# Kernel optimization log

Hardware: AMD Instinct MI355X
Metric: run time of the kernel (lower is better)

Reference implementation:

```python
import jax, jax.numpy as jnp
import numpy as np

C_ATOM, C_Z, N_HEADS = 512, 64, 16
HEAD_DIM = C_ATOM // N_HEADS
EPS = 1e-5


def _layernorm(x, gamma, beta):
    mu = jnp.mean(x, axis=-1, keepdims=True)
    var = jnp.mean(jnp.square(x - mu), axis=-1, keepdims=True)
    return (x - mu) * jax.lax.rsqrt(var + EPS) * gamma + beta


def _adaln(x, cond, gamma, beta, pw, pb):
    # cond: [B, C] -> scale/shift: [B, 1, C]
    ss = cond @ pw.T + pb  # [B, 2C]
    scale, shift = jnp.split(ss[:, None, :], 2, axis=-1)
    return _layernorm(x, gamma, beta) * (1.0 + scale) + shift


def setup_inputs() -> dict:
    key = jax.random.key(0)
    ks = jax.random.split(key, 20)
    B, L = 2, 1024
    s = 1.0 / np.sqrt(C_ATOM)
    inp = {
        "x": jax.random.normal(ks[0], (B, L, C_ATOM), jnp.float32),
        "pair": jax.random.normal(ks[1], (B, L, L, C_Z), jnp.float32),
        "time_cond": jax.random.normal(ks[2], (B, C_ATOM), jnp.float32),
        "ln1_g": jnp.ones((C_ATOM,), jnp.float32),
        "ln1_b": jnp.zeros((C_ATOM,), jnp.float32),
        "ada1_w": jax.random.normal(ks[3], (2 * C_ATOM, C_ATOM), jnp.float32) * 0.02,
        "ada1_b": jnp.zeros((2 * C_ATOM,), jnp.float32),
        "wq": jax.random.normal(ks[4], (C_ATOM, C_ATOM), jnp.float32) * s,
        "wk": jax.random.normal(ks[5], (C_ATOM, C_ATOM), jnp.float32) * s,
        "wv": jax.random.normal(ks[6], (C_ATOM, C_ATOM), jnp.float32) * s,
        "w_pair": jax.random.normal(ks[7], (N_HEADS, C_Z), jnp.float32) * (1.0 / np.sqrt(C_Z)),
        "wo": jax.random.normal(ks[8], (C_ATOM, C_ATOM), jnp.float32) * s,
        "bo": jnp.zeros((C_ATOM,), jnp.float32),
        "ln2_g": jnp.ones((C_ATOM,), jnp.float32),
        "ln2_b": jnp.zeros((C_ATOM,), jnp.float32),
        "ada2_w": jax.random.normal(ks[9], (2 * C_ATOM, C_ATOM), jnp.float32) * 0.02,
        "ada2_b": jnp.zeros((2 * C_ATOM,), jnp.float32),
        "w1": jax.random.normal(ks[10], (4 * C_ATOM, C_ATOM), jnp.float32) * s,
        "b1": jnp.zeros((4 * C_ATOM,), jnp.float32),
        "w2": jax.random.normal(ks[11], (C_ATOM, 4 * C_ATOM), jnp.float32) * (1.0 / np.sqrt(4 * C_ATOM)),
        "b2": jnp.zeros((C_ATOM,), jnp.float32),
    }
    return inp


def reference(x, pair, time_cond, ln1_g, ln1_b, ada1_w, ada1_b, wq, wk, wv,
              w_pair, wo, bo, ln2_g, ln2_b, ada2_w, ada2_b, w1, b1, w2, b2):
    B, L, C = x.shape
    h = _adaln(x, time_cond, ln1_g, ln1_b, ada1_w, ada1_b)
    q = (h @ wq.T).reshape(B, L, N_HEADS, HEAD_DIM)
    k = (h @ wk.T).reshape(B, L, N_HEADS, HEAD_DIM)
    v = (h @ wv.T).reshape(B, L, N_HEADS, HEAD_DIM)
    attn = jnp.einsum('bihd,bjhd->bhij', q, k) / np.sqrt(HEAD_DIM)
    attn = attn + jnp.einsum('bijc,hc->bhij', pair, w_pair)  # additive pair bias
    attn = jax.nn.softmax(attn, axis=-1)
    out = jnp.einsum('bhij,bjhd->bihd', attn, v).reshape(B, L, C)
    x = x + out @ wo.T + bo
    h2 = _adaln(x, time_cond, ln2_g, ln2_b, ada2_w, ada2_b)
    ffn = jax.nn.gelu(h2 @ w1.T + b1, approximate=False) @ w2.T + b2
    return x + ffn
```

## Files before the change

### kernel.cpp

```cpp
#include <hip/hip_runtime.h>
#include <math.h>

typedef unsigned short u16;
typedef __attribute__((ext_vector_type(8))) short bf16x8;
typedef __attribute__((ext_vector_type(4))) short s16x4;
typedef __attribute__((ext_vector_type(4))) float f32x4;

__device__ __forceinline__ u16 f2bf(float f) {
  union { float f; unsigned u; } v; v.f = f;
  unsigned r = v.u + 0x7FFFu + ((v.u >> 16) & 1u);
  return (u16)(r >> 16);
}
__device__ __forceinline__ float bf2f(u16 h) {
  union { unsigned u; float f; } v; v.u = ((unsigned)h) << 16; return v.f;
}
__device__ __forceinline__ void gload_lds16(const void* g, void* l) {
  __builtin_amdgcn_global_load_lds((const __attribute__((address_space(1))) void*)g,
                                   (__attribute__((address_space(3))) void*)l, 16, 0, 0);
}

__global__ __launch_bounds__(256) void k_pre(
    const float* __restrict__ wq, const float* __restrict__ wk,
    const float* __restrict__ wv, const float* __restrict__ wo,
    const float* __restrict__ w1, const float* __restrict__ w2,
    u16* __restrict__ qkvw, u16* __restrict__ wo_bf,
    u16* __restrict__ w1_bf, u16* __restrict__ w2_bf,
    const float* __restrict__ tc,
    const float* __restrict__ wa, const float* __restrict__ ba,
    const float* __restrict__ wb, const float* __restrict__ bb,
    float* __restrict__ ss1, float* __restrict__ ss2) {
  if (blockIdx.x < 3072) {
    int i = (blockIdx.x * 256 + threadIdx.x) * 4;
    const float* s; u16* d;
    if (i < 786432) {
      d = qkvw + i;
      if (i < 262144) s = wq + i;
      else if (i < 524288) s = wk + (i - 262144);
      else s = wv + (i - 524288);
    } else if (i < 1048576) { s = wo + (i - 786432); d = wo_bf + (i - 786432); }
    else if (i < 2097152)   { s = w1 + (i - 1048576); d = w1_bf + (i - 1048576); }
    else                    { s = w2 + (i - 2097152); d = w2_bf + (i - 2097152); }
    float4 v = *(const float4*)s;
    s16x4 o;
    o[0] = (short)f2bf(v.x); o[1] = (short)f2bf(v.y);
    o[2] = (short)f2bf(v.z); o[3] = (short)f2bf(v.w);
    *(s16x4*)d = o;
  } else {
    int wv_ = (blockIdx.x - 3072) * 4 + (threadIdx.x >> 6);
    int l = threadIdx.x & 63;
    int which = wv_ >> 11;
    int rem = wv_ & 2047;
    int b = rem >> 10;
    int row = rem & 1023;
    const float* w = which ? wb : wa;
    const float4* t4 = (const float4*)(tc + b * 512);
    const float4* w4 = (const float4*)(w + (size_t)row * 512);
    float s = 0.f;
#pragma unroll
    for (int q = 0; q < 2; ++q) {
      float4 a = t4[l * 2 + q], c = w4[l * 2 + q];
      s += a.x * c.x + a.y * c.y + a.z * c.z + a.w * c.w;
    }
#pragma unroll
    for (int m = 32; m; m >>= 1) s += __shfl_xor(s, m);
    if (l == 0) {
      float bias = (which ? bb : ba)[row];
      (which ? ss2 : ss1)[b * 1024 + row] = s + bias;
    }
  }
}

__global__ __launch_bounds__(256) void k_adaln(const float* __restrict__ x,
    const float* __restrict__ g, const float* __restrict__ be,
    const float* __restrict__ ss, u16* __restrict__ out) {
  int r = blockIdx.x * 4 + (threadIdx.x >> 6);
  int l = threadIdx.x & 63;
  int b = r >> 10;
  const float4* x4 = (const float4*)(x + (size_t)r * 512);
  float4 v0 = x4[l * 2], v1 = x4[l * 2 + 1];
  float s = v0.x + v0.y + v0.z + v0.w + v1.x + v1.y + v1.z + v1.w;
  float s2 = v0.x*v0.x + v0.y*v0.y + v0.z*v0.z + v0.w*v0.w
           + v1.x*v1.x + v1.y*v1.y + v1.z*v1.z + v1.w*v1.w;
#pragma unroll
  for (int m = 32; m; m >>= 1) { s += __shfl_xor(s, m); s2 += __shfl_xor(s2, m); }
  float mu = s * (1.f / 512.f);
  float var = s2 * (1.f / 512.f) - mu * mu;
  float rstd = rsqrtf(var + 1e-5f);
  int c = l * 8;
  float4 g0 = *(const float4*)(g + c),  g1 = *(const float4*)(g + c + 4);
  float4 e0 = *(const float4*)(be + c), e1 = *(const float4*)(be + c + 4);
  const float* sb = ss + b * 1024;
  float4 sc0 = *(const float4*)(sb + c),       sc1 = *(const float4*)(sb + c + 4);
  float4 sh0 = *(const float4*)(sb + 512 + c), sh1 = *(const float4*)(sb + 512 + c + 4);
  float xe[8] = {v0.x,v0.y,v0.z,v0.w,v1.x,v1.y,v1.z,v1.w};
  float gg[8] = {g0.x,g0.y,g0.z,g0.w,g1.x,g1.y,g1.z,g1.w};
  float ee[8] = {e0.x,e0.y,e0.z,e0.w,e1.x,e1.y,e1.z,e1.w};
  float sc[8] = {sc0.x,sc0.y,sc0.z,sc0.w,sc1.x,sc1.y,sc1.z,sc1.w};
  float sh[8] = {sh0.x,sh0.y,sh0.z,sh0.w,sh1.x,sh1.y,sh1.z,sh1.w};
  bf16x8 o;
#pragma unroll
  for (int e = 0; e < 8; ++e) {
    float hv = (xe[e] - mu) * rstd * gg[e] + ee[e];
    float res = hv * (1.f + sc[e]) + sh[e];
    o[e] = (short)f2bf(res);
  }
  *(bf16x8*)(out + (size_t)r * 512 + c) = o;
}

template<int MODE, int BM, int BN>
__device__ __forceinline__ void gemm_body(
    int bxn, int bxm,
    const u16* __restrict__ A, const u16* __restrict__ Bw,
    int M, int N, int K,
    u16* __restrict__ obf, float* __restrict__ of,
    const float* __restrict__ cb, const float* __restrict__ add_,
    float qscale) {
  constexpr int FM = BM / 32, FN = BN / 32;
  constexpr int WM = BM / 2,  WN = BN / 2;
  __shared__ u16 la[BM * 64];
  __shared__ u16 lb[BN * 64];
  const int tid = threadIdx.x;
  const int l = tid & 63, w = tid >> 6;
  const int wr = w >> 1, wc = w & 1;
  const int m0 = bxm * BM, n0 = bxn * BN;
  f32x4 acc[FM][FN];
  const f32x4 fz = {0.f, 0.f, 0.f, 0.f};
#pragma unroll
  for (int m = 0; m < FM; ++m)
#pragma unroll
    for (int n = 0; n < FN; ++n) acc[m][n] = fz;
  const int nkt = K >> 6;
  for (int kt = 0; kt < nkt; ++kt) {
    const int k0 = kt * 64;
    __syncthreads();
#pragma unroll
    for (int r2 = 0; r2 < BM / 32; ++r2) {
      unsigned e = r2 * 256 + tid;
      unsigned row = e >> 3, ch = (e & 7) ^ (row & 7);
      gload_lds16(A + (size_t)(m0 + row) * K + k0 + ch * 8, la + (e & ~63u) * 8);
    }
#pragma unroll
    for (int r2 = 0; r2 < BN / 32; ++r2) {
      unsigned e = r2 * 256 + tid;
      unsigned row = e >> 3, ch = (e & 7) ^ (row & 7);
      gload_lds16(Bw + (size_t)(n0 + row) * K + k0 + ch * 8, lb + (e & ~63u) * 8);
    }
    __syncthreads();
#pragma unroll
    for (int kk = 0; kk < 2; ++kk) {
      bf16x8 af[FM], bfr[FN];
#pragma unroll
      for (int m = 0; m < FM; ++m) {
        int R = wr * WM + m * 16 + (l & 15);
        int ch = (kk * 4 + (l >> 4)) ^ (R & 7);
        af[m] = *(const bf16x8*)(la + R * 64 + ch * 8);
      }
#pragma unroll
      for (int n = 0; n < FN; ++n) {
        int R = wc * WN + n * 16 + (l & 15);
        int ch = (kk * 4 + (l >> 4)) ^ (R & 7);
        bfr[n] = *(const bf16x8*)(lb + R * 64 + ch * 8);
      }
#pragma unroll
      for (int m = 0; m < FM; ++m)
#pragma unroll
        for (int n = 0; n < FN; ++n)
          acc[m][n] = __builtin_amdgcn_mfma_f32_16x16x32_bf16(af[m], bfr[n], acc[m][n], 0, 0, 0);
    }
  }
  const int rb  = m0 + wr * WM + ((l >> 4) * 4);
  const int cb0 = n0 + wc * WN + (l & 15);
#pragma unroll
  for (int m = 0; m < FM; ++m)
#pragma unroll
    for (int n = 0; n < FN; ++n) {
      int gcol = cb0 + n * 16;
#pragma unroll
      for (int j = 0; j < 4; ++j) {
        int grow = rb + m * 16 + j;
        float v = acc[m][n][j];
        if (MODE == 0) {
          float scv = (gcol < 512) ? qscale : 1.f;
          obf[(size_t)grow * N + gcol] = f2bf(v * scv);
        } else if (MODE == 1) {
          of[(size_t)grow * N + gcol] = v + cb[gcol] + add_[(size_t)grow * N + gcol];
        } else {
          float t = v + cb[gcol];
          float ge = 0.5f * t * (1.f + erff(t * 0.70710678118654752f));
          obf[(size_t)grow * N + gcol] = f2bf(ge);
        }
      }
    }
}

template<int MODE, int BM, int BN>
__global__ __launch_bounds__(256) void k_gemm(
    const u16* __restrict__ A, const u16* __restrict__ Bw,
    int M, int N, int K,
    u16* __restrict__ obf, float* __restrict__ of,
    const float* __restrict__ cb, const float* __restrict__ add_,
    float qscale) {
  gemm_body<MODE, BM, BN>(blockIdx.x, blockIdx.y, A, Bw, M, N, K, obf, of, cb, add_, qscale);
}

__global__ __launch_bounds__(512, 2) void k_fab3(const u16* __restrict__ qkv,
    const float* __restrict__ pair, const float* __restrict__ wp,
    float* __restrict__ opart, float* __restrict__ ml) {
  __shared__ u16 vt[8][64 * 64];
  __shared__ u16 bt[16][16 * 68];
  __shared__ u16 pl[8][2][16 * 64];
  const int tid = threadIdx.x, l = tid & 63, w = tid >> 6;
  const int g = l >> 4, ln = l & 15;
  const int i0 = blockIdx.x * 16;
  const int b  = blockIdx.y;
  const int q  = blockIdx.z;
  const int jt0 = q * 8;
  const u16* base = qkv + (size_t)b * 1024 * 1536;
  const f32x4 fz = {0.f, 0.f, 0.f, 0.f};
  bf16x8 wf[2];
#pragma unroll
  for (int kk = 0; kk < 2; ++kk) {
    const float* wb = wp + ln * 64 + kk * 32 + g * 8;
    float4 w0 = *(const float4*)(wb);
    float4 w1 = *(const float4*)(wb + 4);
    bf16x8 bb;
    bb[0] = (short)f2bf(w0.x); bb[1] = (short)f2bf(w0.y);
    bb[2] = (short)f2bf(w0.z); bb[3] = (short)f2bf(w0.w);
    bb[4] = (short)f2bf(w1.x); bb[5] = (short)f2bf(w1.y);
    bb[6] = (short)f2bf(w1.z); bb[7] = (short)f2bf(w1.w);
    wf[kk] = bb;
  }
  bf16x8 qb[2];
#pragma unroll
  for (int hh = 0; hh < 2; ++hh)
    qb[hh] = *(const bf16x8*)(base + (size_t)(i0 + ln) * 1536 + (w * 2 + hh) * 32 + g * 8);
  float mr[2] = {-1e30f, -1e30f}, ls[2] = {0.f, 0.f};
  f32x4 oa[2][2];
  oa[0][0] = fz; oa[0][1] = fz; oa[1][0] = fz; oa[1][1] = fz;

  auto PF = [&](float4 (&pf)[4][2][2], int ii, int jj0) {
    const float* prow = pair + ((size_t)(b * 1024 + i0 + w * 2 + ii) * 1024 + jj0) * 64;
#pragma unroll
    for (int jf = 0; jf < 4; ++jf)
#pragma unroll
      for (int kk = 0; kk < 2; ++kk) {
        const float* pp = prow + (jf * 16 + ln) * 64 + kk * 32 + g * 8;
        pf[jf][kk][0] = *(const float4*)(pp);
        pf[jf][kk][1] = *(const float4*)(pp + 4);
      }
  };
  auto CONSUME = [&](float4 (&pf)[4][2][2], int ii) {
#pragma unroll
    for (int jf = 0; jf < 4; ++jf) {
      f32x4 ab = fz;
#pragma unroll
      for (int kk = 0; kk < 2; ++kk) {
        float4 p0 = pf[jf][kk][0], p1 = pf[jf][kk][1];
        bf16x8 pk;
        pk[0] = (short)f2bf(p0.x); pk[1] = (short)f2bf(p0.y);
        pk[2] = (short)f2bf(p0.z); pk[3] = (short)f2bf(p0.w);
        pk[4] = (short)f2bf(p1.x); pk[5] = (short)f2bf(p1.y);
        pk[6] = (short)f2bf(p1.z); pk[7] = (short)f2bf(p1.w);
        ab = __builtin_amdgcn_mfma_f32_16x16x32_bf16(pk, wf[kk], ab, 0, 0, 0);
      }
      s16x4 ov;
      ov[0] = (short)f2bf(ab[0]); ov[1] = (short)f2bf(ab[1]);
      ov[2] = (short)f2bf(ab[2]); ov[3] = (short)f2bf(ab[3]);
      *(s16x4*)(&bt[ln][(w * 2 + ii) * 68 + jf * 16 + g * 4]) = ov;
    }
  };

  float4 pfA[4][2][2], pfB[4][2][2];
  PF(pfA, 0, jt0 * 64);
  for (int jt = jt0; jt < jt0 + 8; ++jt) {
    const int j0 = jt * 64;
    __syncthreads();
    PF(pfB, 1, j0);
    CONSUME(pfA, 0);
    CONSUME(pfB, 1);
    if (jt + 1 < jt0 + 8) PF(pfA, 0, j0 + 64);
    {
      const u16* vrow = base + (size_t)(j0 + l) * 1536 + 1024 + w * 64;
      bf16x8 vv[8];
#pragma unroll
      for (int qd = 0; qd < 8; ++qd) vv[qd] = *(const bf16x8*)(vrow + qd * 8);
#pragma unroll
      for (int qd = 0; qd < 8; ++qd)
#pragma unroll
        for (int e = 0; e < 8; ++e) {
          int d = qd * 8 + e;
          vt[w][d * 64 + (l ^ ((d & 7) << 3))] = (u16)vv[qd][e];
        }
    }
    __syncthreads();
#pragma unroll
    for (int hh = 0; hh < 2; ++hh) {
      const int h = w * 2 + hh;
      f32x4 s[4];
#pragma unroll
      for (int jf = 0; jf < 4; ++jf) {
        bf16x8 ak = *(const bf16x8*)(base + (size_t)(j0 + jf * 16 + ln) * 1536 + 512 + h * 32 + g * 8);
        s[jf] = __builtin_amdgcn_mfma_f32_16x16x32_bf16(ak, qb[hh], fz, 0, 0, 0);
      }
#pragma unroll
      for (int jf = 0; jf < 4; ++jf) {
        s16x4 bv = *(const s16x4*)(&bt[h][ln * 68 + jf * 16 + g * 4]);
        s[jf][0] += bf2f((u16)bv[0]);
        s[jf][1] += bf2f((u16)bv[1]);
        s[jf][2] += bf2f((u16)bv[2]);
        s[jf][3] += bf2f((u16)bv[3]);
      }
      float rm = s[0][0];
#pragma unroll
      for (int jf = 0; jf < 4; ++jf)
#pragma unroll
        for (int r = 0; r < 4; ++r) rm = fmaxf(rm, s[jf][r]);
      rm = fmaxf(rm, __shfl_xor(rm, 16));
      rm = fmaxf(rm, __shfl_xor(rm, 32));
      float mn = fmaxf(mr[hh], rm);
      float corr = __expf(mr[hh] - mn);
      float p[4][4];
      float rs = 0.f;
#pragma unroll
      for (int jf = 0; jf < 4; ++jf)
#pragma unroll
        for (int r = 0; r < 4; ++r) { p[jf][r] = __expf(s[jf][r] - mn); rs += p[jf][r]; }
      rs += __shfl_xor(rs, 16);
      rs += __shfl_xor(rs, 32);
      ls[hh] = ls[hh] * corr + rs;
      mr[hh] = mn;
      u16* plw = &pl[w][hh][0];
#pragma unroll
      for (int jf = 0; jf < 4; ++jf) {
        s16x4 pv;
        pv[0] = (short)f2bf(p[jf][0]); pv[1] = (short)f2bf(p[jf][1]);
        pv[2] = (short)f2bf(p[jf][2]); pv[3] = (short)f2bf(p[jf][3]);
        *(s16x4*)(plw + ln * 64 + ((jf * 16 + g * 4) ^ ((ln & 7) << 3))) = pv;
      }
      float cr[4];
#pragma unroll
      for (int r = 0; r < 4; ++r) cr[r] = __shfl(corr, g * 4 + r, 16);
#pragma unroll
      for (int nf = 0; nf < 2; ++nf) {
        oa[hh][nf][0] *= cr[0]; oa[hh][nf][1] *= cr[1];
        oa[hh][nf][2] *= cr[2]; oa[hh][nf][3] *= cr[3];
      }
#pragma unroll
      for (int kk = 0; kk < 2; ++kk) {
        bf16x8 pa = *(const bf16x8*)(plw + ln * 64 + ((kk * 32 + g * 8) ^ ((ln & 7) << 3)));
#pragma unroll
        for (int nf = 0; nf < 2; ++nf) {
          int dp = hh * 32 + nf * 16 + ln;
          bf16x8 vb = *(const bf16x8*)(&vt[w][dp * 64 + ((kk * 32 + g * 8) ^ ((dp & 7) << 3))]);
          oa[hh][nf] = __builtin_amdgcn_mfma_f32_16x16x32_bf16(pa, vb, oa[hh][nf], 0, 0, 0);
        }
      }
    }
  }
  float* op = opart + (size_t)q * 1048576;
#pragma unroll
  for (int hh = 0; hh < 2; ++hh) {
    const int h = w * 2 + hh;
    if (g == 0) {
      float2* mlp = (float2*)ml;
      mlp[(size_t)q * 32768 + (size_t)(b * 1024 + i0 + ln) * 16 + h] =
          make_float2(mr[hh], ls[hh]);
    }
#pragma unroll
    for (int nf = 0; nf < 2; ++nf)
#pragma unroll
      for (int r = 0; r < 4; ++r) {
        int m = g * 4 + r;
        op[(size_t)(b * 1024 + i0 + m) * 512 + h * 32 + nf * 16 + ln] = oa[hh][nf][r];
      }
  }
}

__global__ __launch_bounds__(256) void k_merge(const float* __restrict__ opart,
    const float* __restrict__ ml, u16* __restrict__ ob) {
  int gid = blockIdx.x * 256 + threadIdx.x;
  int row = gid >> 7;
  int d4  = (gid & 127) * 4;
  int h   = d4 >> 5;
  const float2* mlp = (const float2*)ml;
  float2 a = mlp[(size_t)row * 16 + h];
  float2 c = mlp[32768 + (size_t)row * 16 + h];
  float mx = fmaxf(a.x, c.x);
  float w0 = __expf(a.x - mx), w1 = __expf(c.x - mx);
  float inv = 1.f / (a.y * w0 + c.y * w1);
  float4 o0 = *(const float4*)(opart + (size_t)row * 512 + d4);
  float4 o1 = *(const float4*)(opart + 1048576 + (size_t)row * 512 + d4);
  s16x4 o;
  o[0] = (short)f2bf((o0.x * w0 + o1.x * w1) * inv);
  o[1] = (short)f2bf((o0.y * w0 + o1.y * w1) * inv);
  o[2] = (short)f2bf((o0.z * w0 + o1.z * w1) * inv);
  o[3] = (short)f2bf((o0.w * w0 + o1.w * w1) * inv);
  *(s16x4*)(ob + (size_t)row * 512 + d4) = o;
}

extern "C" void kernel_launch(void* const* d_in, const int* in_sizes, int n_in,
                              void* d_out, int out_size, void* d_ws, size_t ws_size,
                              hipStream_t stream) {
  const float* x    = (const float*)d_in[0];
  const float* pair = (const float*)d_in[1];
  const float* tc   = (const float*)d_in[2];
  const float* ln1g = (const float*)d_in[3];
  const float* ln1b = (const float*)d_in[4];
  const float* a1w  = (const float*)d_in[5];
  const float* a1b  = (const float*)d_in[6];
  const float* wq   = (const float*)d_in[7];
  const float* wk   = (const float*)d_in[8];
  const float* wv   = (const float*)d_in[9];
  const float* wp   = (const float*)d_in[10];
  const float* wo   = (const float*)d_in[11];
  const float* bo   = (const float*)d_in[12];
  const float* ln2g = (const float*)d_in[13];
  const float* ln2b = (const float*)d_in[14];
  const float* a2w  = (const float*)d_in[15];
  const float* a2b  = (const float*)d_in[16];
  const float* w1   = (const float*)d_in[17];
  const float* b1   = (const float*)d_in[18];
  const float* w2   = (const float*)d_in[19];
  const float* b2   = (const float*)d_in[20];
  float* out = (float*)d_out;

  char* ws = (char*)d_ws;
  size_t off = 0;
  auto alloc = [&](size_t bytes) {
    size_t cur = off;
    off += (bytes + 255) & ~(size_t)255;
    return (void*)(ws + cur);
  };
  float* ss1    = (float*)alloc(2 * 1024 * 4);
  float* ss2    = (float*)alloc(2 * 1024 * 4);
  u16*   qkvw   = (u16*)alloc((size_t)1536 * 512 * 2);
  u16*   wo_bf  = (u16*)alloc((size_t)512 * 512 * 2);
  u16*   w1_bf  = (u16*)alloc((size_t)2048 * 512 * 2);
  u16*   w2_bf  = (u16*)alloc((size_t)512 * 2048 * 2);
  u16*   h_bf   = (u16*)alloc((size_t)2048 * 512 * 2);
  u16*   qkv_bf = (u16*)alloc((size_t)2048 * 1536 * 2);
  u16*   o_bf   = (u16*)alloc((size_t)2048 * 512 * 2);
  u16*   h2_bf  = (u16*)alloc((size_t)2048 * 512 * 2);
  float* xmid   = (float*)alloc((size_t)2048 * 512 * 4);
  u16*   mid_bf = (u16*)alloc((size_t)2048 * 2048 * 2);
  float* opart  = (float*)alloc((size_t)2 * 2048 * 512 * 4);
  float* mlbuf  = (float*)alloc((size_t)2 * 2048 * 16 * 8);
  (void)ws_size; (void)in_sizes; (void)n_in; (void)out_size;

  k_pre<<<4096, 256, 0, stream>>>(wq, wk, wv, wo, w1, w2,
                                  qkvw, wo_bf, w1_bf, w2_bf,
                                  tc, a1w, a1b, a2w, a2b, ss1, ss2);

  k_adaln<<<512, 256, 0, stream>>>(x, ln1g, ln1b, ss1, h_bf);

  k_gemm<0, 64, 128><<<dim3(12, 32), 256, 0, stream>>>(h_bf, qkvw, 2048, 1536, 512,
      qkv_bf, nullptr, nullptr, nullptr, 0.17677669529663687f);

  k_fab3<<<dim3(64, 2, 2), 512, 0, stream>>>(qkv_bf, pair, wp, opart, mlbuf);

  k_merge<<<1024, 256, 0, stream>>>(opart, mlbuf, o_bf);

  k_gemm<1, 64, 64><<<dim3(8, 32), 256, 0, stream>>>(o_bf, wo_bf, 2048, 512, 512,
      nullptr, xmid, bo, x, 1.f);

  k_adaln<<<512, 256, 0, stream>>>(xmid, ln2g, ln2b, ss2, h2_bf);

  k_gemm<2, 64, 128><<<dim3(16, 32), 256, 0, stream>>>(h2_bf, w1_bf, 2048, 2048, 512,
      mid_bf, nullptr, b1, nullptr, 1.f);

  k_gemm<1, 64, 64><<<dim3(8, 32), 256, 0, stream>>>(mid_bf, w2_bf, 2048, 512, 2048,
      nullptr, out, b2, xmid, 1.f);
}
```

Baseline: 223.8 us.

## Fuse split-softmax merge into output-projection GEMM and store partials as bf16

Removes the separate k_merge kernel. The two attention partial outputs are now combined with their softmax max/sum weights inside the A-tile load of the Wo GEMM (new MODE 3). The partial outputs are also stored as bf16 instead of fp32, which halves that intermediate traffic. In exchange the A tile goes through synchronous register loads and LDS stores instead of direct global-to-LDS loads, and the extra rounding of the unnormalised partials before the merge adds some precision loss.

```diff
diff --git a/kernel.cpp b/kernel.cpp
--- a/kernel.cpp
+++ b/kernel.cpp
@@ -114,7 +114,7 @@
     int M, int N, int K,
     u16* __restrict__ obf, float* __restrict__ of,
     const float* __restrict__ cb, const float* __restrict__ add_,
-    float qscale) {
+    float qscale, const float* __restrict__ mlb) {
   constexpr int FM = BM / 32, FN = BN / 32;
   constexpr int WM = BM / 2,  WN = BN / 2;
   __shared__ u16 la[BM * 64];
@@ -137,7 +137,30 @@
     for (int r2 = 0; r2 < BM / 32; ++r2) {
       unsigned e = r2 * 256 + tid;
       unsigned row = e >> 3, ch = (e & 7) ^ (row & 7);
-      gload_lds16(A + (size_t)(m0 + row) * K + k0 + ch * 8, la + (e & ~63u) * 8);
+      if (MODE == 3) {
+        int grow = m0 + (int)row;
+        int kbase = k0 + (int)ch * 8;
+        int h = kbase >> 5;
+        const u16* p0 = A + (size_t)grow * 512 + kbase;
+        const u16* p1 = A + 1048576 + (size_t)grow * 512 + kbase;
+        s16x4 q00 = *(const s16x4*)p0, q01 = *(const s16x4*)(p0 + 4);
+        s16x4 q10 = *(const s16x4*)p1, q11 = *(const s16x4*)(p1 + 4);
+        const float2* mlp = (const float2*)mlb;
+        float2 ma = mlp[(size_t)grow * 16 + h];
+        float2 mc = mlp[32768 + (size_t)grow * 16 + h];
+        float mx = fmaxf(ma.x, mc.x);
+        float w0 = __expf(ma.x - mx), w1 = __expf(mc.x - mx);
+        float inv = 1.f / (ma.y * w0 + mc.y * w1);
+        bf16x8 ov;
+#pragma unroll
+        for (int j = 0; j < 4; ++j) {
+          ov[j]     = (short)f2bf((bf2f((u16)q00[j]) * w0 + bf2f((u16)q10[j]) * w1) * inv);
+          ov[j + 4] = (short)f2bf((bf2f((u16)q01[j]) * w0 + bf2f((u16)q11[j]) * w1) * inv);
+        }
+        *(bf16x8*)(la + e * 8) = ov;
+      } else {
+        gload_lds16(A + (size_t)(m0 + row) * K + k0 + ch * 8, la + (e & ~63u) * 8);
+      }
     }
 #pragma unroll
     for (int r2 = 0; r2 < BN / 32; ++r2) {
@@ -182,7 +205,7 @@
         if (MODE == 0) {
           float scv = (gcol < 512) ? qscale : 1.f;
           obf[(size_t)grow * N + gcol] = f2bf(v * scv);
-        } else if (MODE == 1) {
+        } else if (MODE == 1 || MODE == 3) {
           of[(size_t)grow * N + gcol] = v + cb[gcol] + add_[(size_t)grow * N + gcol];
         } else {
           float t = v + cb[gcol];
@@ -199,13 +222,14 @@
     int M, int N, int K,
     u16* __restrict__ obf, float* __restrict__ of,
     const float* __restrict__ cb, const float* __restrict__ add_,
-    float qscale) {
-  gemm_body<MODE, BM, BN>(blockIdx.x, blockIdx.y, A, Bw, M, N, K, obf, of, cb, add_, qscale);
+    float qscale, const float* __restrict__ mlb) {
+  gemm_body<MODE, BM, BN>(blockIdx.x, blockIdx.y, A, Bw, M, N, K, obf, of, cb, add_,
+                          qscale, mlb);
 }
 
 __global__ __launch_bounds__(512, 2) void k_fab3(const u16* __restrict__ qkv,
     const float* __restrict__ pair, const float* __restrict__ wp,
-    float* __restrict__ opart, float* __restrict__ ml) {
+    u16* __restrict__ opart, float* __restrict__ ml) {
   __shared__ u16 vt[8][64 * 64];
   __shared__ u16 bt[16][16 * 68];
   __shared__ u16 pl[8][2][16 * 64];
@@ -357,7 +381,7 @@
       }
     }
   }
-  float* op = opart + (size_t)q * 1048576;
+  u16* op = opart + (size_t)q * 1048576;
 #pragma unroll
   for (int hh = 0; hh < 2; ++hh) {
     const int h = w * 2 + hh;
@@ -371,31 +395,9 @@
 #pragma unroll
       for (int r = 0; r < 4; ++r) {
         int m = g * 4 + r;
-        op[(size_t)(b * 1024 + i0 + m) * 512 + h * 32 + nf * 16 + ln] = oa[hh][nf][r];
-      }
-  }
-}
-
-__global__ __launch_bounds__(256) void k_merge(const float* __restrict__ opart,
-    const float* __restrict__ ml, u16* __restrict__ ob) {
-  int gid = blockIdx.x * 256 + threadIdx.x;
-  int row = gid >> 7;
-  int d4  = (gid & 127) * 4;
-  int h   = d4 >> 5;
-  const float2* mlp = (const float2*)ml;
-  float2 a = mlp[(size_t)row * 16 + h];
-  float2 c = mlp[32768 + (size_t)row * 16 + h];
-  float mx = fmaxf(a.x, c.x);
-  float w0 = __expf(a.x - mx), w1 = __expf(c.x - mx);
-  float inv = 1.f / (a.y * w0 + c.y * w1);
-  float4 o0 = *(const float4*)(opart + (size_t)row * 512 + d4);
-  float4 o1 = *(const float4*)(opart + 1048576 + (size_t)row * 512 + d4);
-  s16x4 o;
-  o[0] = (short)f2bf((o0.x * w0 + o1.x * w1) * inv);
-  o[1] = (short)f2bf((o0.y * w0 + o1.y * w1) * inv);
-  o[2] = (short)f2bf((o0.z * w0 + o1.z * w1) * inv);
-  o[3] = (short)f2bf((o0.w * w0 + o1.w * w1) * inv);
-  *(s16x4*)(ob + (size_t)row * 512 + d4) = o;
+        op[(size_t)(b * 1024 + i0 + m) * 512 + h * 32 + nf * 16 + ln] = f2bf(oa[hh][nf][r]);
+      }
+  }
 }
 
 extern "C" void kernel_launch(void* const* d_in, const int* in_sizes, int n_in,
@@ -439,11 +441,10 @@
   u16*   w2_bf  = (u16*)alloc((size_t)512 * 2048 * 2);
   u16*   h_bf   = (u16*)alloc((size_t)2048 * 512 * 2);
   u16*   qkv_bf = (u16*)alloc((size_t)2048 * 1536 * 2);
-  u16*   o_bf   = (u16*)alloc((size_t)2048 * 512 * 2);
   u16*   h2_bf  = (u16*)alloc((size_t)2048 * 512 * 2);
   float* xmid   = (float*)alloc((size_t)2048 * 512 * 4);
   u16*   mid_bf = (u16*)alloc((size_t)2048 * 2048 * 2);
-  float* opart  = (float*)alloc((size_t)2 * 2048 * 512 * 4);
+  u16*   opart  = (u16*)alloc((size_t)2 * 2048 * 512 * 2);
   float* mlbuf  = (float*)alloc((size_t)2 * 2048 * 16 * 8);
   (void)ws_size; (void)in_sizes; (void)n_in; (void)out_size;
 
@@ -454,20 +455,18 @@
   k_adaln<<<512, 256, 0, stream>>>(x, ln1g, ln1b, ss1, h_bf);
 
   k_gemm<0, 64, 128><<<dim3(12, 32), 256, 0, stream>>>(h_bf, qkvw, 2048, 1536, 512,
-      qkv_bf, nullptr, nullptr, nullptr, 0.17677669529663687f);
+      qkv_bf, nullptr, nullptr, nullptr, 0.17677669529663687f, nullptr);
 
   k_fab3<<<dim3(64, 2, 2), 512, 0, stream>>>(qkv_bf, pair, wp, opart, mlbuf);
 
-  k_merge<<<1024, 256, 0, stream>>>(opart, mlbuf, o_bf);
-
-  k_gemm<1, 64, 64><<<dim3(8, 32), 256, 0, stream>>>(o_bf, wo_bf, 2048, 512, 512,
-      nullptr, xmid, bo, x, 1.f);
+  k_gemm<3, 64, 64><<<dim3(8, 32), 256, 0, stream>>>(opart, wo_bf, 2048, 512, 512,
+      nullptr, xmid, bo, x, 1.f, mlbuf);
 
   k_adaln<<<512, 256, 0, stream>>>(xmid, ln2g, ln2b, ss2, h2_bf);
 
   k_gemm<2, 64, 128><<<dim3(16, 32), 256, 0, stream>>>(h2_bf, w1_bf, 2048, 2048, 512,
-      mid_bf, nullptr, b1, nullptr, 1.f);
+      mid_bf, nullptr, b1, nullptr, 1.f, nullptr);
 
   k_gemm<1, 64, 64><<<dim3(8, 32), 256, 0, stream>>>(mid_bf, w2_bf, 2048, 512, 2048,
-      nullptr, out, b2, xmid, 1.f);
-}
+      nullptr, out, b2, xmid, 1.f, nullptr);
+}
```

Result: no change. 224.2 us (+0.2%).
